# Performance work log

Hardware: AMD Instinct MI355X
Metric: run time of the kernel (lower is better)

The kernel has to match this reference:

```python
import jax, jax.numpy as jnp
import numpy as np

N = 20000      # nodes
E = 200000     # edges (before self loops)
H = 8          # heads
C = 256        # out_channels per head
IN = 256       # in_channels
OUT = 250      # final linear out


def setup_inputs() -> dict:
    key = jax.random.key(0)
    ks = jax.random.split(key, 8)
    x = jax.random.normal(ks[0], (N, IN), jnp.float32)
    edge_index = jax.random.randint(ks[1], (2, E), 0, N)
    # GATConv params (lin has no bias in PyG; bias is on the conv output)
    W_gat = jax.random.normal(ks[2], (IN, H * C), jnp.float32) * 0.02
    att_src = jax.random.normal(ks[3], (H, C), jnp.float32) * 0.1
    att_dst = jax.random.normal(ks[4], (H, C), jnp.float32) * 0.1
    b_gat = jnp.zeros((H * C,), jnp.float32)
    # conv1: 1x1 conv with 1 in/out channel -> scalar weight + scalar bias
    conv_w = jax.random.normal(ks[5], (), jnp.float32)
    conv_b = jnp.zeros((), jnp.float32)
    W_lin = jax.random.normal(ks[6], (C, OUT), jnp.float32) * 0.02
    b_lin = jnp.zeros((OUT,), jnp.float32)
    return dict(x=x, edge_index=edge_index, W_gat=W_gat, att_src=att_src,
                att_dst=att_dst, b_gat=b_gat, conv_w=conv_w, conv_b=conv_b,
                W_lin=W_lin, b_lin=b_lin)


def reference(x, edge_index, W_gat, att_src, att_dst, b_gat, conv_w, conv_b, W_lin, b_lin):
    # --- GATConv (PyG defaults: add_self_loops=True, negative_slope=0.2, concat=True) ---
    loops = jnp.arange(N)
    src = jnp.concatenate([edge_index[0], loops])  # [E+N]
    dst = jnp.concatenate([edge_index[1], loops])
    xh = (x @ W_gat).reshape(N, H, C)              # [N,H,C]
    a_s = jnp.einsum('nhc,hc->nh', xh, att_src)    # [N,H]
    a_d = jnp.einsum('nhc,hc->nh', xh, att_dst)
    e = jax.nn.leaky_relu(a_s[src] + a_d[dst], 0.2)  # [E+N, H]
    # segment softmax over edges sharing a destination node
    m = jax.ops.segment_max(e, dst, num_segments=N)
    m = jnp.where(jnp.isfinite(m), m, 0.0)
    ex = jnp.exp(e - m[dst])
    s = jax.ops.segment_sum(ex, dst, num_segments=N)
    alpha = ex / (s[dst] + 1e-16)                  # [E+N, H]
    msg = xh[src] * alpha[:, :, None]              # [E+N, H, C]  (dominant traffic)
    agg = jax.ops.segment_sum(msg, dst, num_segments=N)  # [N,H,C]
    agg = agg + b_gat.reshape(H, C)
    # --- head split / pool / 1x1 conv / head softmax / fuse ---
    z = agg.transpose(1, 0, 2)                     # [H,N,C]  (torch z is [H,1,N,C])
    pooled = z.mean(axis=(1, 2))                   # [H] global avg pool
    g = jax.nn.relu(pooled * conv_w + conv_b)
    w = jax.nn.softmax(g, axis=0)                  # softmax over heads (dim=0)
    fuse = jnp.einsum('hnc,h->nc', z, w)           # sum over heads of z * w
    Hf = jax.nn.relu(fuse + x)                     # residual with input features
    return Hf @ W_lin + b_lin                      # [N, 250]
```

## Files before the change

### kernel.cpp

```cpp
#include <hip/hip_runtime.h>
#include <hip/hip_bf16.h>


typedef __attribute__((ext_vector_type(8))) short short8v;
typedef __attribute__((ext_vector_type(4))) float float4v;

__device__ __forceinline__ unsigned f2bfu(float f) {
  unsigned u = __float_as_uint(f);
  return (u + 0x7fffu + ((u >> 16) & 1u)) >> 16;
}
__device__ __forceinline__ float bfu_lo(unsigned u) { return __uint_as_float(u << 16); }
__device__ __forceinline__ float bfu_hi(unsigned u) { return __uint_as_float(u & 0xffff0000u); }
__device__ __forceinline__ unsigned pack2(float a, float b) { return f2bfu(a) | (f2bfu(b) << 16); }

__device__ __forceinline__ void ld8(const float* p, float* v) {
  float4 a = ((const float4*)p)[0], b = ((const float4*)p)[1];
  v[0] = a.x; v[1] = a.y; v[2] = a.z; v[3] = a.w;
  v[4] = b.x; v[5] = b.y; v[6] = b.z; v[7] = b.w;
}

__device__ __forceinline__ float bcast(float x, int e) {
  return __uint_as_float((unsigned)__builtin_amdgcn_readlane((int)__float_as_uint(x), e));
}

__device__ __forceinline__ void gll16(const void* g, void* l) {
  __builtin_amdgcn_global_load_lds(
      (__attribute__((address_space(1))) void*)const_cast<void*>(g),
      (__attribute__((address_space(3))) void*)(l), 16, 0, 0);
}

__global__ __launch_bounds__(256) void prep1_kernel(
    const float* __restrict__ W_lin, short* __restrict__ wlT,
    const float* __restrict__ W, const float* __restrict__ att_s,
    const float* __restrict__ att_d, float* __restrict__ ws_s,
    float* __restrict__ ws_d, float* __restrict__ ws_r,
    const int* __restrict__ ei, int* __restrict__ deg) {
  __shared__ float smem[4096];
  int b = blockIdx.x;
  int t = threadIdx.x;
  if (b < 64) {
    float (*tile)[33] = (float(*)[33])smem;
    int tx = t & 31, ty = t >> 5;
    int c0 = (b & 7) * 32, r0 = (b >> 3) * 32;
    #pragma unroll
    for (int j = ty; j < 32; j += 8) {
      int r = r0 + j, c = c0 + tx;
      tile[j][tx] = (c < 250) ? W_lin[(size_t)r * 250 + c] : 0.f;
    }
    __syncthreads();
    #pragma unroll
    for (int j = ty; j < 32; j += 8) {
      int c = c0 + j, r = r0 + tx;
      wlT[(size_t)c * 256 + r] = (short)f2bfu(tile[tx][j]);
    }
  } else if (b < 96) {
    float* sas = smem;
    float* sad = smem + 2048;
    for (int i = t; i < 2048; i += 256) { sas[i] = att_s[i]; sad[i] = att_d[i]; }
    __syncthreads();
    int kk = t >> 5, h = (t >> 2) & 7, q = t & 3;
    int k = (b - 64) * 8 + kk;
    const float4* wr = (const float4*)(W + (size_t)k * 2048 + h * 256 + q * 64);
    const float* as = sas + h * 256 + q * 64;
    const float* ad = sad + h * 256 + q * 64;
    float s = 0.f, dd = 0.f, r = 0.f;
    #pragma unroll
    for (int c4 = 0; c4 < 16; ++c4) {
      float4 wv = wr[c4];
      int c = c4 * 4;
      s  += wv.x * as[c] + wv.y * as[c + 1] + wv.z * as[c + 2] + wv.w * as[c + 3];
      dd += wv.x * ad[c] + wv.y * ad[c + 1] + wv.z * ad[c + 2] + wv.w * ad[c + 3];
      r  += wv.x + wv.y + wv.z + wv.w;
    }
    #pragma unroll
    for (int off = 1; off < 4; off <<= 1) {
      s += __shfl_xor(s, off);
      dd += __shfl_xor(dd, off);
      r += __shfl_xor(r, off);
    }
    if (q == 0) {
      int g = k * 8 + h;
      ws_s[g] = s;
      ws_d[g] = dd;
      ws_r[g] = r;
    }
  } else {
    int e = (b - 96) * 256 + t;
    if (e < 200000) atomicAdd(&deg[ei[200000 + e]], 1);
  }
}

__global__ __launch_bounds__(256) void asd_kernel(const float* __restrict__ x,
    const float* __restrict__ ws_s, const float* __restrict__ ws_d,
    float* __restrict__ a_s, float* __restrict__ a_d, short* __restrict__ x_bf) {
  __shared__ float ls[2048], ld2[2048];
  int tid = threadIdx.x;
  for (int i = tid; i < 2048; i += 256) { ls[i] = ws_s[i]; ld2[i] = ws_d[i]; }
  __syncthreads();
  int node = blockIdx.x * 32 + (tid >> 3);
  int h = tid & 7;
  const float4* xr = (const float4*)(x + (size_t)node * 256);
  float as = 0.f, ad = 0.f;
  #pragma unroll 1
  for (int g = 0; g < 8; ++g) {
    bool own = (g == h);
    int bufi[16];
    #pragma unroll
    for (int j = 0; j < 8; ++j) {
      int k4 = g * 8 + j;
      float4 v = xr[k4];
      int k8 = k4 * 32 + h;
      as += v.x * ls[k8] + v.y * ls[k8 + 8] + v.z * ls[k8 + 16] + v.w * ls[k8 + 24];
      ad += v.x * ld2[k8] + v.y * ld2[k8 + 8] + v.z * ld2[k8 + 16] + v.w * ld2[k8 + 24];
      bufi[2 * j] = (int)pack2(v.x, v.y);
      bufi[2 * j + 1] = (int)pack2(v.z, v.w);
    }
    if (own) {
      int4* dst = (int4*)(x_bf + (size_t)node * 256 + h * 32);
      dst[0] = make_int4(bufi[0], bufi[1], bufi[2], bufi[3]);
      dst[1] = make_int4(bufi[4], bufi[5], bufi[6], bufi[7]);
      dst[2] = make_int4(bufi[8], bufi[9], bufi[10], bufi[11]);
      dst[3] = make_int4(bufi[12], bufi[13], bufi[14], bufi[15]);
    }
  }
  a_s[node * 8 + h] = as;
  a_d[node * 8 + h] = ad;
}

__global__ __launch_bounds__(256, 2) void gemm_fused_kernel(
    const short* __restrict__ u, const short* __restrict__ wmixT,
    const short* __restrict__ wlT, short* __restrict__ Hf,
    float* __restrict__ out, const float* __restrict__ fb,
    const float* __restrict__ x, const float* __restrict__ b_lin, int M) {
  __shared__ short lA[64 * 128];
  __shared__ short lB[256 * 128];
  int tid = threadIdx.x;
  int wave = tid >> 6, lane = tid & 63;
  int m0 = blockIdx.x << 6;
  int lr = lane & 15, lq = lane >> 4;
  int lrow4 = lane >> 4;
  int pch = lane & 15;

  float4v acc[4][4];
  #pragma unroll
  for (int i = 0; i < 4; ++i)
    #pragma unroll
    for (int j = 0; j < 4; ++j) acc[i][j] = (float4v){0.f, 0.f, 0.f, 0.f};

  int rowlA[4], growA[4], logA[4];
  #pragma unroll
  for (int it = 0; it < 4; ++it) {
    rowlA[it] = wave * 16 + it * 4 + lrow4;
    int grow = m0 + rowlA[it];
    if (grow >= M) grow = M - 1;
    growA[it] = grow;
    logA[it] = pch ^ (rowlA[it] & 7);
  }
  int rowB[16], logB[16];
  #pragma unroll
  for (int it = 0; it < 16; ++it) {
    rowB[it] = wave * 64 + it * 4 + lrow4;
    logB[it] = pch ^ (rowB[it] & 7);
  }

  for (int t = 0; t < 16; ++t) {
    int k0 = t << 7;
    __syncthreads();
    #pragma unroll
    for (int it = 0; it < 4; ++it)
      gll16(u + (size_t)growA[it] * 2048 + logA[it] * 8 + k0, lA + (wave * 16 + it * 4) * 128);
    #pragma unroll
    for (int it = 0; it < 16; ++it)
      gll16(wmixT + (size_t)rowB[it] * 2048 + logB[it] * 8 + k0, lB + (wave * 64 + it * 4) * 128);
    __syncthreads();
    #pragma unroll
    for (int ks = 0; ks < 4; ++ks) {
      int phys = ((ks * 4 + lq) ^ (lr & 7)) * 8;
      short8v af[4], bfv[4];
      #pragma unroll
      for (int i = 0; i < 4; ++i)
        af[i] = *(const short8v*)(lA + (i * 16 + lr) * 128 + phys);
      #pragma unroll
      for (int j = 0; j < 4; ++j)
        bfv[j] = *(const short8v*)(lB + (wave * 64 + j * 16 + lr) * 128 + phys);
      #pragma unroll
      for (int i = 0; i < 4; ++i)
        #pragma unroll
        for (int j = 0; j < 4; ++j)
          acc[i][j] = __builtin_amdgcn_mfma_f32_16x16x32_bf16(af[i], bfv[j], acc[i][j], 0, 0, 0);
    }
  }
  #pragma unroll
  for (int i = 0; i < 4; ++i) {
    #pragma unroll
    for (int jj = 0; jj < 4; ++jj) {
      int row = m0 + i * 16 + lq * 4 + jj;
      if (row >= M) continue;
      #pragma unroll
      for (int j = 0; j < 4; ++j) {
        int col = wave * 64 + j * 16 + lr;
        float o = acc[i][j][jj] + fb[col] + x[(size_t)row * 256 + col];
        Hf[(size_t)row * 256 + col] = (short)f2bfu(fmaxf(o, 0.f));
      }
    }
  }

  #pragma unroll
  for (int i = 0; i < 4; ++i)
    #pragma unroll
    for (int j = 0; j < 4; ++j) acc[i][j] = (float4v){0.f, 0.f, 0.f, 0.f};

  for (int t = 0; t < 2; ++t) {
    int k0 = t << 7;
    __syncthreads();
    #pragma unroll
    for (int it = 0; it < 4; ++it)
      gll16(Hf + (size_t)growA[it] * 256 + logA[it] * 8 + k0, lA + (wave * 16 + it * 4) * 128);
    #pragma unroll
    for (int it = 0; it < 16; ++it)
      gll16(wlT + (size_t)rowB[it] * 256 + logB[it] * 8 + k0, lB + (wave * 64 + it * 4) * 128);
    __syncthreads();
    #pragma unroll
    for (int ks = 0; ks < 4; ++ks) {
      int phys = ((ks * 4 + lq) ^ (lr & 7)) * 8;
      short8v af[4], bfv[4];
      #pragma unroll
      for (int i = 0; i < 4; ++i)
        af[i] = *(const short8v*)(lA + (i * 16 + lr) * 128 + phys);
      #pragma unroll
      for (int j = 0; j < 4; ++j)
        bfv[j] = *(const short8v*)(lB + (wave * 64 + j * 16 + lr) * 128 + phys);
      #pragma unroll
      for (int i = 0; i < 4; ++i)
        #pragma unroll
        for (int j = 0; j < 4; ++j)
          acc[i][j] = __builtin_amdgcn_mfma_f32_16x16x32_bf16(af[i], bfv[j], acc[i][j], 0, 0, 0);
    }
  }
  #pragma unroll
  for (int i = 0; i < 4; ++i) {
    #pragma unroll
    for (int jj = 0; jj < 4; ++jj) {
      int row = m0 + i * 16 + lq * 4 + jj;
      if (row >= M) continue;
      #pragma unroll
      for (int j = 0; j < 4; ++j) {
        int col = wave * 64 + j * 16 + lr;
        if (col < 250) out[(size_t)row * 250 + col] = acc[i][j][jj] + b_lin[col];
      }
    }
  }
}


__global__ __launch_bounds__(1024) void scan_kernel(const int* __restrict__ deg,
                                                    int* __restrict__ rowptr,
                                                    int* __restrict__ cursor, int n) {
  __shared__ int part[1024];
  int t = threadIdx.x;
  int base = t * 20;
  int loc[20];
  int run = 0;
  #pragma unroll
  for (int j = 0; j < 20; ++j) {
    int idx = base + j;
    int v = (idx < n) ? deg[idx] : 0;
    loc[j] = run;
    run += v;
  }
  part[t] = run;
  __syncthreads();
  for (int off = 1; off < 1024; off <<= 1) {
    int add = (t >= off) ? part[t - off] : 0;
    __syncthreads();
    part[t] += add;
    __syncthreads();
  }
  int off0 = (t > 0) ? part[t - 1] : 0;
  #pragma unroll
  for (int j = 0; j < 20; ++j) {
    int idx = base + j;
    if (idx < n) {
      int v = off0 + loc[j];
      rowptr[idx] = v;
      cursor[idx] = v;
    }
  }
  if (t == 1023) rowptr[n] = part[1023];
}

__global__ void scatter_kernel(const int* __restrict__ ei, int* __restrict__ cursor,
                               int* __restrict__ csr_src, int E) {
  int e = blockIdx.x * 256 + threadIdx.x;
  if (e < E) {
    int pos = atomicAdd(&cursor[ei[E + e]], 1);
    csr_src[pos] = ei[e];
  }
}

__global__ __launch_bounds__(256) void alphaz_kernel(
    const short* __restrict__ x_bf, const float* __restrict__ a_s,
    const float* __restrict__ a_d, const float* __restrict__ ws_r,
    const int* __restrict__ rowptr, const int* __restrict__ csr,
    short* __restrict__ u, float* __restrict__ pp) {
  int d = blockIdx.x * 4 + (threadIdx.x >> 6);
  int lane = threadIdx.x & 63;
  int cl = lane * 4;
  int beg = rowptr[d];
  int deg = rowptr[d + 1] - beg;
  int nb = deg + 1;

  float ad8[8];
  ld8(a_d + (size_t)d * 8, ad8);

  float acc[8][4];
  #pragma unroll
  for (int h = 0; h < 8; ++h)
    #pragma unroll
    for (int c = 0; c < 4; ++c) acc[h][c] = 0.f;
  float s8[8] = {0, 0, 0, 0, 0, 0, 0, 0};

  for (int base = 0; base < nb; base += 64) {
    int i = base + lane;
    bool act = i < nb;
    int srcv = d;
    if (i < deg) srcv = csr[beg + i];
    float ex[8];
    {
      float t8[8];
      ld8(a_s + (size_t)srcv * 8, t8);
      #pragma unroll
      for (int h = 0; h < 8; ++h) {
        float e = t8[h] + ad8[h];
        e = (e > 0.f) ? e : 0.2f * e;
        float xx = act ? __expf(e) : 0.f;
        ex[h] = xx;
        s8[h] += xx;
      }
    }
    int cnt = nb - base;
    if (cnt > 64) cnt = 64;
    for (int e = 0; e < cnt; ++e) {
      int sb = __builtin_amdgcn_readlane(srcv, e);
      uint2 v = *(const uint2*)(x_bf + (size_t)sb * 256 + cl);
      float q[8];
      #pragma unroll
      for (int h = 0; h < 8; ++h) q[h] = bcast(ex[h], e);
      float xv0 = bfu_lo(v.x), xv1 = bfu_hi(v.x);
      float xv2 = bfu_lo(v.y), xv3 = bfu_hi(v.y);
      #pragma unroll
      for (int h = 0; h < 8; ++h) {
        acc[h][0] += q[h] * xv0;
        acc[h][1] += q[h] * xv1;
        acc[h][2] += q[h] * xv2;
        acc[h][3] += q[h] * xv3;
      }
    }
  }

  #pragma unroll
  for (int off = 1; off < 64; off <<= 1)
    #pragma unroll
    for (int h = 0; h < 8; ++h) s8[h] += __shfl_xor(s8[h], off);
  float inv[8];
  #pragma unroll
  for (int h = 0; h < 8; ++h) inv[h] = 1.f / (s8[h] + 1e-16f);

  #pragma unroll
  for (int h = 0; h < 8; ++h) {
    uint2 ov;
    ov.x = pack2(acc[h][0] * inv[h], acc[h][1] * inv[h]);
    ov.y = pack2(acc[h][2] * inv[h], acc[h][3] * inv[h]);
    *(uint2*)(u + (size_t)d * 2048 + h * 256 + cl) = ov;
  }

  float ppl[8] = {0, 0, 0, 0, 0, 0, 0, 0};
  {
    const float4* wr = (const float4*)(ws_r + (size_t)cl * 8);
    #pragma unroll
    for (int c = 0; c < 4; ++c) {
      float4 wa = wr[c * 2], wb = wr[c * 2 + 1];
      float zc[8];
      #pragma unroll
      for (int h = 0; h < 8; ++h) zc[h] = acc[h][c] * inv[h];
      ppl[0] += zc[0] * wa.x; ppl[1] += zc[1] * wa.y;
      ppl[2] += zc[2] * wa.z; ppl[3] += zc[3] * wa.w;
      ppl[4] += zc[4] * wb.x; ppl[5] += zc[5] * wb.y;
      ppl[6] += zc[6] * wb.z; ppl[7] += zc[7] * wb.w;
    }
  }
  #pragma unroll
  for (int off = 1; off < 64; off <<= 1)
    #pragma unroll
    for (int h = 0; h < 8; ++h) ppl[h] += __shfl_xor(ppl[h], off);
  if (lane == 0) {
    ((float4*)(pp + (size_t)d * 8))[0] = make_float4(ppl[0], ppl[1], ppl[2], ppl[3]);
    ((float4*)(pp + (size_t)d * 8))[1] = make_float4(ppl[4], ppl[5], ppl[6], ppl[7]);
  }
}

__global__ __launch_bounds__(256) void reduce_pp_kernel(const float* __restrict__ pp,
                                                        float* __restrict__ pooled) {
  int tid = threadIdx.x;
  float loc[8] = {0, 0, 0, 0, 0, 0, 0, 0};
  for (int r = blockIdx.x * 256 + tid; r < 20000; r += 80 * 256) {
    float t[8];
    ld8(pp + (size_t)r * 8, t);
    #pragma unroll
    for (int h = 0; h < 8; ++h) loc[h] += t[h];
  }
  #pragma unroll
  for (int off = 1; off < 64; off <<= 1)
    #pragma unroll
    for (int h = 0; h < 8; ++h) loc[h] += __shfl_xor(loc[h], off);
  __shared__ float sred[4][8];
  int wave = tid >> 6, lane = tid & 63;
  if (lane == 0) {
    #pragma unroll
    for (int h = 0; h < 8; ++h) sred[wave][h] = loc[h];
  }
  __syncthreads();
  if (tid < 8) {
    atomicAdd(&pooled[tid], sred[0][tid] + sred[1][tid] + sred[2][tid] + sred[3][tid]);
  }
}

__global__ __launch_bounds__(256) void headwfb_kernel(const float* __restrict__ pooled,
    const float* __restrict__ b_gat, const float* __restrict__ conv_w,
    const float* __restrict__ conv_b, float* __restrict__ wsoft,
    float* __restrict__ fb) {
  __shared__ float sb[8];
  __shared__ float sw[8];
  int t = threadIdx.x;
  float v = 0.f;
  #pragma unroll
  for (int j = 0; j < 8; ++j) v += b_gat[t * 8 + j];
  #pragma unroll
  for (int off = 1; off < 32; off <<= 1) v += __shfl_xor(v, off);
  if ((t & 31) == 0) sb[t >> 5] = v;
  __syncthreads();
  if (t == 0) {
    const float invNC = 1.0f / (20000.0f * 256.0f);
    float g[8];
    float mx = -1e30f;
    #pragma unroll
    for (int h = 0; h < 8; ++h) {
      float pm = (pooled[h] + 20000.0f * sb[h]) * invNC;
      float gv = pm * conv_w[0] + conv_b[0];
      gv = fmaxf(gv, 0.f);
      g[h] = gv;
      mx = fmaxf(mx, gv);
    }
    float ssum = 0.f;
    #pragma unroll
    for (int h = 0; h < 8; ++h) { g[h] = __expf(g[h] - mx); ssum += g[h]; }
    #pragma unroll
    for (int h = 0; h < 8; ++h) {
      float w = g[h] / ssum;
      wsoft[h] = w;
      sw[h] = w;
    }
  }
  __syncthreads();
  float a = 0.f;
  #pragma unroll
  for (int h = 0; h < 8; ++h) a += sw[h] * b_gat[h * 256 + t];
  fb[t] = a;
}

__global__ void wmix_kernel(const float* __restrict__ W, const float* __restrict__ wsoft,
                            short* __restrict__ out) {
  __shared__ float tile[32][33];
  int tx = threadIdx.x, ty = threadIdx.y;
  int h = blockIdx.z;
  float wh = wsoft[h];
  int c0 = blockIdx.x * 32, k0 = blockIdx.y * 32;
  #pragma unroll
  for (int j = ty; j < 32; j += 8)
    tile[j][tx] = W[(size_t)(k0 + j) * 2048 + h * 256 + c0 + tx];
  __syncthreads();
  #pragma unroll
  for (int j = ty; j < 32; j += 8)
    out[(size_t)(c0 + j) * 2048 + h * 256 + k0 + tx] = (short)f2bfu(wh * tile[tx][j]);
}

extern "C" void kernel_launch(void* const* d_in, const int* in_sizes, int n_in,
                              void* d_out, int out_size, void* d_ws, size_t ws_size,
                              hipStream_t stream) {
  (void)in_sizes; (void)n_in; (void)out_size; (void)ws_size;
  const float* x      = (const float*)d_in[0];
  const int*   ei     = (const int*)d_in[1];
  const float* W_gat  = (const float*)d_in[2];
  const float* att_s  = (const float*)d_in[3];
  const float* att_d  = (const float*)d_in[4];
  const float* b_gat  = (const float*)d_in[5];
  const float* conv_w = (const float*)d_in[6];
  const float* conv_b = (const float*)d_in[7];
  const float* W_lin  = (const float*)d_in[8];
  const float* b_lin  = (const float*)d_in[9];
  float* out = (float*)d_out;

  char* p = (char*)d_ws;
  size_t off = 0;
  auto alloc = [&](size_t bytes) -> void* {
    void* r = p + off;
    off = (off + bytes + 255) & ~(size_t)255;
    return r;
  };
  short* x_bf   = (short*)alloc((size_t)20000 * 256 * 2);
  short* wmixT  = (short*)alloc((size_t)256 * 2048 * 2);
  short* wlT    = (short*)alloc((size_t)256 * 256 * 2);
  float* ws_s   = (float*)alloc(2048 * 4);
  float* ws_d   = (float*)alloc(2048 * 4);
  float* ws_r   = (float*)alloc(2048 * 4);
  float* a_s    = (float*)alloc((size_t)20000 * 8 * 4);
  float* a_d    = (float*)alloc((size_t)20000 * 8 * 4);
  int*   deg    = (int*)alloc(20000 * 4);
  float* pooled = (float*)alloc(8 * 4);
  float* wsoft  = (float*)alloc(8 * 4);
  float* fb     = (float*)alloc(256 * 4);
  int*   rowptr = (int*)alloc(20001 * 4);
  int*   cursor = (int*)alloc(20000 * 4);
  int*   csr    = (int*)alloc(200000 * 4);
  float* pp     = (float*)alloc((size_t)20000 * 8 * 4);
  short* u      = (short*)alloc((size_t)20000 * 2048 * 2);
  short* Hf     = x_bf;

  hipMemsetAsync(deg, 0, 20000 * 4, stream);
  hipMemsetAsync(pooled, 0, 8 * 4, stream);

  prep1_kernel<<<878, 256, 0, stream>>>(W_lin, wlT, W_gat, att_s, att_d,
                                        ws_s, ws_d, ws_r, ei, deg);
  scan_kernel<<<1, 1024, 0, stream>>>(deg, rowptr, cursor, 20000);
  asd_kernel<<<625, 256, 0, stream>>>(x, ws_s, ws_d, a_s, a_d, x_bf);
  scatter_kernel<<<782, 256, 0, stream>>>(ei, cursor, csr, 200000);
  alphaz_kernel<<<5000, 256, 0, stream>>>(x_bf, a_s, a_d, ws_r, rowptr, csr, u, pp);
  reduce_pp_kernel<<<80, 256, 0, stream>>>(pp, pooled);
  headwfb_kernel<<<1, 256, 0, stream>>>(pooled, b_gat, conv_w, conv_b, wsoft, fb);
  wmix_kernel<<<dim3(8, 8, 8), dim3(32, 8), 0, stream>>>(W_gat, wsoft, wmixT);
  gemm_fused_kernel<<<313, 256, 0, stream>>>(u, wmixT, wlT, Hf, out, fb, x, b_lin, 20000);
}
```

Measured before the change: 194.4 us.

## Split fused dual GEMM into two templated 64x64-tile GEMM launches

Replaces the single fused kernel, which computed a 64x256 output tile with a 128-wide K step and then ran the second GEMM in the same block, with a generic templated GEMM that uses 64x64 tiles and 32-wide K steps. The generic GEMM is launched twice, once for the mix GEMM with a residual/relu/bf16 epilogue and once for the final linear. The aim is more blocks (1280 versus 313) and higher occupancy (launch bounds 4), with block indices swizzled so that neighbouring blocks share A rows. In exchange, A is now re-read once per N tile, Hf makes a round trip through global memory between two launches, and the much smaller K step means more barriers per MFMA.

```diff
diff --git a/kernel.cpp b/kernel.cpp
--- a/kernel.cpp
+++ b/kernel.cpp
@@ -127,126 +127,77 @@
   a_d[node * 8 + h] = ad;
 }
 
-__global__ __launch_bounds__(256, 2) void gemm_fused_kernel(
-    const short* __restrict__ u, const short* __restrict__ wmixT,
-    const short* __restrict__ wlT, short* __restrict__ Hf,
-    float* __restrict__ out, const float* __restrict__ fb,
-    const float* __restrict__ x, const float* __restrict__ b_lin, int M) {
-  __shared__ short lA[64 * 128];
-  __shared__ short lB[256 * 128];
+template <int EPI>
+__global__ __launch_bounds__(256, 4) void gemm_kernel(
+    const short* __restrict__ A, const short* __restrict__ BT,
+    int M, int K,
+    short* __restrict__ Cb, float* __restrict__ Cf,
+    const float* __restrict__ bias, const float* __restrict__ xres, int Nout) {
+  int g = blockIdx.x;
+  int xk = g & 7, tt = g >> 3;
+  int it = xk + 8 * (tt >> 2);
+  if (it >= ((M + 63) >> 6)) return;
+  int m0 = it << 6;
+  int n0 = (tt & 3) << 6;
+
+  __shared__ short lA[64 * 32];
+  __shared__ short lB[64 * 32];
   int tid = threadIdx.x;
   int wave = tid >> 6, lane = tid & 63;
-  int m0 = blockIdx.x << 6;
+  int wm = wave >> 1, wn = wave & 1;
   int lr = lane & 15, lq = lane >> 4;
-  int lrow4 = lane >> 4;
-  int pch = lane & 15;
-
-  float4v acc[4][4];
-  #pragma unroll
-  for (int i = 0; i < 4; ++i)
-    #pragma unroll
-    for (int j = 0; j < 4; ++j) acc[i][j] = (float4v){0.f, 0.f, 0.f, 0.f};
-
-  int rowlA[4], growA[4], logA[4];
-  #pragma unroll
-  for (int it = 0; it < 4; ++it) {
-    rowlA[it] = wave * 16 + it * 4 + lrow4;
-    int grow = m0 + rowlA[it];
-    if (grow >= M) grow = M - 1;
-    growA[it] = grow;
-    logA[it] = pch ^ (rowlA[it] & 7);
-  }
-  int rowB[16], logB[16];
-  #pragma unroll
-  for (int it = 0; it < 16; ++it) {
-    rowB[it] = wave * 64 + it * 4 + lrow4;
-    logB[it] = pch ^ (rowB[it] & 7);
-  }
-
-  for (int t = 0; t < 16; ++t) {
-    int k0 = t << 7;
-    __syncthreads();
-    #pragma unroll
-    for (int it = 0; it < 4; ++it)
-      gll16(u + (size_t)growA[it] * 2048 + logA[it] * 8 + k0, lA + (wave * 16 + it * 4) * 128);
-    #pragma unroll
-    for (int it = 0; it < 16; ++it)
-      gll16(wmixT + (size_t)rowB[it] * 2048 + logB[it] * 8 + k0, lB + (wave * 64 + it * 4) * 128);
-    __syncthreads();
-    #pragma unroll
-    for (int ks = 0; ks < 4; ++ks) {
-      int phys = ((ks * 4 + lq) ^ (lr & 7)) * 8;
-      short8v af[4], bfv[4];
-      #pragma unroll
-      for (int i = 0; i < 4; ++i)
-        af[i] = *(const short8v*)(lA + (i * 16 + lr) * 128 + phys);
-      #pragma unroll
-      for (int j = 0; j < 4; ++j)
-        bfv[j] = *(const short8v*)(lB + (wave * 64 + j * 16 + lr) * 128 + phys);
-      #pragma unroll
-      for (int i = 0; i < 4; ++i)
-        #pragma unroll
-        for (int j = 0; j < 4; ++j)
-          acc[i][j] = __builtin_amdgcn_mfma_f32_16x16x32_bf16(af[i], bfv[j], acc[i][j], 0, 0, 0);
-    }
-  }
-  #pragma unroll
-  for (int i = 0; i < 4; ++i) {
+
+  float4v acc[2][2];
+  #pragma unroll
+  for (int i = 0; i < 2; ++i)
+    #pragma unroll
+    for (int j = 0; j < 2; ++j) acc[i][j] = (float4v){0.f, 0.f, 0.f, 0.f};
+
+  int sr = lane >> 2;
+  int sw = (lane >> 3) & 3;
+  int sc = ((lane & 3) ^ sw) << 3;
+  int arow = m0 + wave * 16 + sr;
+  if (arow >= M) arow = M - 1;
+  const short* pA = A + (size_t)arow * K + sc;
+  const short* pB = BT + (size_t)(n0 + wave * 16 + sr) * K + sc;
+
+  int rsw = ((lr >> 1) & 3) ^ lq;
+
+  for (int k0 = 0; k0 < K; k0 += 32) {
+    __syncthreads();
+    gll16(pA + k0, lA + wave * 512);
+    gll16(pB + k0, lB + wave * 512);
+    __syncthreads();
+    short8v af[2], bfv[2];
+    #pragma unroll
+    for (int i = 0; i < 2; ++i)
+      af[i] = *(const short8v*)(lA + (wm * 32 + i * 16 + lr) * 32 + rsw * 8);
+    #pragma unroll
+    for (int j = 0; j < 2; ++j)
+      bfv[j] = *(const short8v*)(lB + (wn * 32 + j * 16 + lr) * 32 + rsw * 8);
+    #pragma unroll
+    for (int i = 0; i < 2; ++i)
+      #pragma unroll
+      for (int j = 0; j < 2; ++j)
+        acc[i][j] = __builtin_amdgcn_mfma_f32_16x16x32_bf16(af[i], bfv[j], acc[i][j], 0, 0, 0);
+  }
+
+  #pragma unroll
+  for (int i = 0; i < 2; ++i) {
     #pragma unroll
     for (int jj = 0; jj < 4; ++jj) {
-      int row = m0 + i * 16 + lq * 4 + jj;
+      int row = m0 + wm * 32 + i * 16 + lq * 4 + jj;
       if (row >= M) continue;
       #pragma unroll
-      for (int j = 0; j < 4; ++j) {
-        int col = wave * 64 + j * 16 + lr;
-        float o = acc[i][j][jj] + fb[col] + x[(size_t)row * 256 + col];
-        Hf[(size_t)row * 256 + col] = (short)f2bfu(fmaxf(o, 0.f));
-      }
-    }
-  }
-
-  #pragma unroll
-  for (int i = 0; i < 4; ++i)
-    #pragma unroll
-    for (int j = 0; j < 4; ++j) acc[i][j] = (float4v){0.f, 0.f, 0.f, 0.f};
-
-  for (int t = 0; t < 2; ++t) {
-    int k0 = t << 7;
-    __syncthreads();
-    #pragma unroll
-    for (int it = 0; it < 4; ++it)
-      gll16(Hf + (size_t)growA[it] * 256 + logA[it] * 8 + k0, lA + (wave * 16 + it * 4) * 128);
-    #pragma unroll
-    for (int it = 0; it < 16; ++it)
-      gll16(wlT + (size_t)rowB[it] * 256 + logB[it] * 8 + k0, lB + (wave * 64 + it * 4) * 128);
-    __syncthreads();
-    #pragma unroll
-    for (int ks = 0; ks < 4; ++ks) {
-      int phys = ((ks * 4 + lq) ^ (lr & 7)) * 8;
-      short8v af[4], bfv[4];
-      #pragma unroll
-      for (int i = 0; i < 4; ++i)
-        af[i] = *(const short8v*)(lA + (i * 16 + lr) * 128 + phys);
-      #pragma unroll
-      for (int j = 0; j < 4; ++j)
-        bfv[j] = *(const short8v*)(lB + (wave * 64 + j * 16 + lr) * 128 + phys);
-      #pragma unroll
-      for (int i = 0; i < 4; ++i)
-        #pragma unroll
-        for (int j = 0; j < 4; ++j)
-          acc[i][j] = __builtin_amdgcn_mfma_f32_16x16x32_bf16(af[i], bfv[j], acc[i][j], 0, 0, 0);
-    }
-  }
-  #pragma unroll
-  for (int i = 0; i < 4; ++i) {
-    #pragma unroll
-    for (int jj = 0; jj < 4; ++jj) {
-      int row = m0 + i * 16 + lq * 4 + jj;
-      if (row >= M) continue;
-      #pragma unroll
-      for (int j = 0; j < 4; ++j) {
-        int col = wave * 64 + j * 16 + lr;
-        if (col < 250) out[(size_t)row * 250 + col] = acc[i][j][jj] + b_lin[col];
+      for (int j = 0; j < 2; ++j) {
+        int col = n0 + wn * 32 + j * 16 + lr;
+        float v = acc[i][j][jj];
+        if (EPI == 1) {
+          if (col < Nout) Cf[(size_t)row * Nout + col] = v + bias[col];
+        } else {
+          float o = v + bias[col] + xres[(size_t)row * 256 + col];
+          Cb[(size_t)row * 256 + col] = (short)f2bfu(fmaxf(o, 0.f));
+        }
       }
     }
   }
@@ -538,5 +489,8 @@
   reduce_pp_kernel<<<80, 256, 0, stream>>>(pp, pooled);
   headwfb_kernel<<<1, 256, 0, stream>>>(pooled, b_gat, conv_w, conv_b, wsoft, fb);
   wmix_kernel<<<dim3(8, 8, 8), dim3(32, 8), 0, stream>>>(W_gat, wsoft, wmixT);
-  gemm_fused_kernel<<<313, 256, 0, stream>>>(u, wmixT, wlT, Hf, out, fb, x, b_lin, 20000);
-}
+  gemm_kernel<2><<<1280, 256, 0, stream>>>(u, wmixT, 20000, 2048,
+                                           Hf, nullptr, fb, x, 256);
+  gemm_kernel<1><<<1280, 256, 0, stream>>>(Hf, wlT, 20000, 256,
+                                           nullptr, out, b_lin, nullptr, 250);
+}
```

After: 186.3 us. 1.04x faster.
